# Optimization experiments

Measured on AMD Instinct MI355X. Metric: run time of the kernel, lower is better.

Reference implementation:

```python
import jax, jax.numpy as jnp
import numpy as np

N_PMTS = 12
N_TICKS = 550
BIN_SIGMA = 0.1
GAUSS_NORM = 1.0 / (BIN_SIGMA * 2.5066282746)
B, N_DEP, K = 8, 64, 512  # batch, depositions/event, electron slot cap per deposition


def setup_inputs() -> dict:
    key = jax.random.key(0)
    ks = jax.random.split(key, 10)
    # energy depositions [B, N, 4] = x, y, z, E(MeV)
    xy = jax.random.normal(ks[0], (B, N_DEP, 2), dtype=jnp.float32) * 5.0
    z = jax.random.uniform(ks[1], (B, N_DEP, 1), dtype=jnp.float32, minval=50.0, maxval=500.0)
    # E ~ 0.0115 MeV -> n = E*1e6/22.4 ~ up to ~513 electrons, capped at K
    E = jax.random.uniform(ks[2], (B, N_DEP, 1), dtype=jnp.float32, minval=0.002, maxval=0.0115)
    energy_depositions = jnp.concatenate([xy, z, E], axis=-1)
    return {
        "energy_depositions": energy_depositions,
        "e_draws": jax.random.normal(ks[3], (B, N_DEP), dtype=jnp.float32),
        "diff_draws": jax.random.normal(ks[4], (B, N_DEP, K, 3), dtype=jnp.float32),
        "unif_draws": jax.random.uniform(ks[5], (B, N_DEP, K), dtype=jnp.float32),
        "W1": jax.random.normal(ks[6], (2, 28), dtype=jnp.float32) * (1.0 / np.sqrt(2.0)),
        "b1": jnp.zeros((28,), dtype=jnp.float32),
        "W2": jax.random.normal(ks[7], (28, 12), dtype=jnp.float32) * (1.0 / np.sqrt(28.0)),
        "b2": jnp.zeros((12,), dtype=jnp.float32),
        "diffusion_scale": jnp.array([1.0, 1.0, 0.25], dtype=jnp.float32),
        "pmt_response_scale": jnp.ones((12,), dtype=jnp.float32),
        "lifetime": jnp.float32(25.0),
    }


def reference(energy_depositions, e_draws, diff_draws, unif_draws,
              W1, b1, W2, b2, diffusion_scale, pmt_response_scale, lifetime):
    dt = energy_depositions.dtype
    pos = energy_depositions[..., :3]            # [B,N,3]
    E = energy_depositions[..., 3]               # [B,N]
    # generate_electrons: n = E*1e6/22.4, sigma = sqrt(0.15 n)
    n = E * 1000.0 * 1000.0 / 22.4
    sigma = jnp.sqrt(0.15 * n)
    n_elec = jnp.clip((sigma * e_draws + n).astype(jnp.int32), 0, K)  # [B,N]
    slot_mask = jnp.arange(K)[None, None, :] < n_elec[..., None]       # [B,N,K]
    # diffuse_electrons: scale^2 * draw * sqrt(z) + position
    sqrt_z = jnp.sqrt(pos[..., 2])                                     # [B,N]
    elec = (diffusion_scale ** 2) * diff_draws * sqrt_z[..., None, None] + pos[:, :, None, :]  # [B,N,K,3]
    z_e = elec[..., 2]                                                 # [B,N,K]
    # apply_lifetime: accept with prob 1 - exp(-z/lifetime)
    prob = 1.0 - jnp.exp(-z_e / lifetime)
    mask = (slot_mask & (prob > unif_draws)).astype(dt)                # [B,N,K]
    # PMT response MLP on xy, scaled
    xy_e = elec[..., :2]
    h = jax.nn.sigmoid(xy_e @ W1 + b1)
    pmt = jax.nn.sigmoid(h @ W2 + b2) * (pmt_response_scale ** 2)      # [B,N,K,12]
    pmt = pmt * mask[..., None]
    # gaussian tick histogram over 550 ticks centered at 0.5..549.5
    ticks = jnp.arange(N_TICKS, dtype=dt) + 0.5
    g = GAUSS_NORM * jnp.exp(-((ticks - z_e[..., None]) ** 2) / BIN_SIGMA)  # [B,N,K,550]
    # sum over all electrons of the event: [B, 12, 550]
    return jnp.einsum('bnkp,bnkt->bpt', pmt, g)
```

## Files before the change

### kernel.cpp

```cpp
#include <hip/hip_runtime.h>
#include <hip/hip_fp16.h>

#define NB   8
#define NDEP 64
#define KK   512
#define NP   12
#define NT   550
#define L2E  1.4426950408889634f


static __device__ __forceinline__ float fast_rcp(float x) {
    return __builtin_amdgcn_rcpf(x);
}
static __device__ __forceinline__ unsigned packh2(float a, float b) {
    __half2 h = __floats2half2_rn(a, b);
    return __builtin_bit_cast(unsigned, h);
}

__global__ __launch_bounds__(256) void init_kernel(
    const float* __restrict__ W1, const float* __restrict__ b1,
    const float* __restrict__ W2, const float* __restrict__ b2,
    const float* __restrict__ pscale,
    float* __restrict__ ws, float* __restrict__ out, int out_size)
{
    const int idx = blockIdx.x * 256 + threadIdx.x;
    for (int i = idx; i < out_size; i += gridDim.x * 256) out[i] = 0.0f;

    if (blockIdx.x == 0) {
        const int t = threadIdx.x;
        if (t < 28) {
            ws[t]      = W1[t]      * L2E;
            ws[28 + t] = W1[28 + t] * L2E;
            ws[56 + t] = b1[t]      * L2E;
        }
        if (t >= 64 && t < 232) {
            const int e = t - 64, j = e / 6, c = e - j * 6;
            ((unsigned*)(ws + 84))[e] = packh2(W2[j * NP + 2 * c], W2[j * NP + 2 * c + 1]);
        }
        if (t >= 232 && t < 238) {
            const int c = t - 232;
            ((unsigned*)(ws + 252))[c] = packh2(b2[2 * c], b2[2 * c + 1]);
        }
        if (t >= 238 && t < 250) {
            const int p = t - 238;
            ws[258 + p] = pscale[p] * pscale[p] * 3.9894228040143274f;
        }
    }
}

template<int S>
static __device__ __forceinline__ void gather_reduce(
    const float* __restrict__ wl, int lane, int t_lo, int b,
    float* __restrict__ out)
{
    constexpr int W = 64 / S;
    const int tw  = lane & (W - 1);
    const int sub = lane / W;
    const float tc = (float)(t_lo + tw) + 0.5f;

    float acc[NP];
    #pragma unroll
    for (int p = 0; p < NP; ++p) acc[p] = 0.0f;

    #pragma unroll 4
    for (int i = 0; i < W; ++i) {
        const int k = sub * W + i;
        const int o = (k << 4) + ((k >> 4) << 2);
        const float4 r0 = *(const float4*)&wl[o];
        const float4 r1 = *(const float4*)&wl[o + 4];
        const float4 r2 = *(const float4*)&wl[o + 8];
        const float ez  = wl[o + 12];
        const float d   = tc - ez;
        const float g   = exp2f(-14.426950408889634f * d * d);
        acc[0]  = fmaf(r0.x, g, acc[0]);  acc[1]  = fmaf(r0.y, g, acc[1]);
        acc[2]  = fmaf(r0.z, g, acc[2]);  acc[3]  = fmaf(r0.w, g, acc[3]);
        acc[4]  = fmaf(r1.x, g, acc[4]);  acc[5]  = fmaf(r1.y, g, acc[5]);
        acc[6]  = fmaf(r1.z, g, acc[6]);  acc[7]  = fmaf(r1.w, g, acc[7]);
        acc[8]  = fmaf(r2.x, g, acc[8]);  acc[9]  = fmaf(r2.y, g, acc[9]);
        acc[10] = fmaf(r2.z, g, acc[10]); acc[11] = fmaf(r2.w, g, acc[11]);
    }

    #pragma unroll
    for (int msk = W; msk < 64; msk <<= 1) {
        #pragma unroll
        for (int p = 0; p < NP; ++p) acc[p] += __shfl_xor(acc[p], msk);
    }

    if (lane < W) {
        float* ob = out + ((size_t)b * NP) * NT + (t_lo + tw);
        #pragma unroll
        for (int p = 0; p < NP; ++p) atomicAdd(&ob[p * NT], acc[p]);
    }
}

__global__ __launch_bounds__(256) void next_sim_wave(
    const float* __restrict__ ed,
    const float* __restrict__ edraw,
    const float* __restrict__ ddraw,
    const float* __restrict__ udraw,
    const float* __restrict__ wst,
    const float* __restrict__ dscale, const float* __restrict__ life,
    float* __restrict__ out)
{
    __shared__ float lds[4][1040];

    const int tid  = threadIdx.x;
    const int lane = tid & 63;
    const int wid  = tid >> 6;
    const int bid  = blockIdx.x;
    const int bn   = bid >> 1;
    const int g    = ((bid & 1) << 2) | wid;
    const int b    = bn >> 6;

    const float4 dep  = ((const float4*)ed)[bn];
    const float nval  = dep.w * (1000000.0f / 22.4f);
    const float sigma = sqrtf(0.15f * nval);
    int ne = (int)(sigma * edraw[bn] + nval);
    ne = min(max(ne, 0), KK);
    const int k0 = g << 6;
    if (k0 >= ne) return;

    const float sqz     = sqrtf(dep.z);
    const float invLife = fast_rcp(life[0]);
    const float dS0 = dscale[0] * dscale[0];
    const float dS1 = dscale[1] * dscale[1];
    const float dS2 = dscale[2] * dscale[2];

    const int k = k0 + lane;
    const float* dd = ddraw + ((size_t)bn * KK + k) * 3;
    const float d0 = dd[0], d1 = dd[1], d2 = dd[2];
    const float ez = fmaf(dS2 * d2, sqz, dep.z);
    const float ex = fmaf(dS0 * d0, sqz, dep.x);
    const float ey = fmaf(dS1 * d1, sqz, dep.y);
    const float prob = 1.0f - __expf(-ez * invLife);
    const float m = ((k < ne) && (prob > udraw[(size_t)bn * KK + k])) ? 1.0f : 0.0f;

    const float*   w1a  = wst;
    const float*   w1b  = wst + 28;
    const float*   b1s  = wst + 56;
    const __half2* w2pk = (const __half2*)(wst + 84);
    const __half2* b2pk = (const __half2*)(wst + 252);
    const float*   qtab = wst + 258;

    __half2 pa0 = b2pk[0], pa1 = b2pk[1], pa2 = b2pk[2];
    __half2 pa3 = b2pk[3], pa4 = b2pk[4], pa5 = b2pk[5];
    #pragma unroll 4
    for (int j = 0; j < 28; ++j) {
        const float lg  = fmaf(w1a[j], ex, fmaf(w1b[j], ey, b1s[j]));
        const float hjf = fast_rcp(1.0f + exp2f(-lg));
        const __half2 h2 = __float2half2_rn(hjf);
        pa0 = __hfma2(h2, w2pk[j * 6 + 0], pa0);
        pa1 = __hfma2(h2, w2pk[j * 6 + 1], pa1);
        pa2 = __hfma2(h2, w2pk[j * 6 + 2], pa2);
        pa3 = __hfma2(h2, w2pk[j * 6 + 3], pa3);
        pa4 = __hfma2(h2, w2pk[j * 6 + 4], pa4);
        pa5 = __hfma2(h2, w2pk[j * 6 + 5], pa5);
    }
    float pm[NP];
    { float2 f;
      f = __half22float2(pa0); pm[0] = f.x; pm[1] = f.y;
      f = __half22float2(pa1); pm[2] = f.x; pm[3] = f.y;
      f = __half22float2(pa2); pm[4] = f.x; pm[5] = f.y;
      f = __half22float2(pa3); pm[6] = f.x; pm[7] = f.y;
      f = __half22float2(pa4); pm[8] = f.x; pm[9] = f.y;
      f = __half22float2(pa5); pm[10] = f.x; pm[11] = f.y; }

    float q[NP];
    #pragma unroll
    for (int p = 0; p < NP; ++p)
        q[p] = qtab[p] * m * fast_rcp(1.0f + exp2f(-pm[p] * L2E));

    float* wl = lds[wid];
    const int off = (lane << 4) + ((lane >> 4) << 2);
    *(float4*)&wl[off]     = make_float4(q[0], q[1],  q[2],  q[3]);
    *(float4*)&wl[off + 4] = make_float4(q[4], q[5],  q[6],  q[7]);
    *(float4*)&wl[off + 8] = make_float4(q[8], q[9],  q[10], q[11]);
    wl[off + 12] = ez;

    float ezmin = ez, ezmax = ez;
    #pragma unroll
    for (int msk = 1; msk < 64; msk <<= 1) {
        ezmin = fminf(ezmin, __shfl_xor(ezmin, msk));
        ezmax = fmaxf(ezmax, __shfl_xor(ezmax, msk));
    }
    const int fmin = (int)floorf(ezmin);
    const int fmax = (int)floorf(ezmax);
    const int need = fmax - fmin + 7;

    if (need <= 16) {
        const int t_lo = min(max(fmin - 3, 0), NT - 16);
        gather_reduce<4>(wl, lane, t_lo, b, out);
    } else {
        const int t_lo = min(max(fmin - 3, 0), NT - 32);
        gather_reduce<2>(wl, lane, t_lo, b, out);
    }
}

extern "C" void kernel_launch(void* const* d_in, const int* in_sizes, int n_in,
                              void* d_out, int out_size, void* d_ws, size_t ws_size,
                              hipStream_t stream) {
    const float* ed     = (const float*)d_in[0];
    const float* edraw  = (const float*)d_in[1];
    const float* ddraw  = (const float*)d_in[2];
    const float* udraw  = (const float*)d_in[3];
    const float* W1     = (const float*)d_in[4];
    const float* b1     = (const float*)d_in[5];
    const float* W2     = (const float*)d_in[6];
    const float* b2     = (const float*)d_in[7];
    const float* dscale = (const float*)d_in[8];
    const float* pscale = (const float*)d_in[9];
    const float* life   = (const float*)d_in[10];
    float* ws  = (float*)d_ws;
    float* out = (float*)d_out;

    init_kernel<<<64, 256, 0, stream>>>(W1, b1, W2, b2, pscale, ws, out, out_size);
    next_sim_wave<<<NB * NDEP * 2, 256, 0, stream>>>(
        ed, edraw, ddraw, udraw, ws, dscale, life, out);
}
```

Before: 20.66 us.

## Reduce per-deposition partials in LDS before global atomics, one block per deposition

```diff
diff --git a/kernel.cpp b/kernel.cpp
--- a/kernel.cpp
+++ b/kernel.cpp
@@ -6,6 +6,7 @@
 #define KK   512
 #define NP   12
 #define NT   550
+#define BWIN 40
 #define L2E  1.4426950408889634f
 
 
@@ -49,14 +50,14 @@
 }
 
 template<int S>
-static __device__ __forceinline__ void gather_reduce(
-    const float* __restrict__ wl, int lane, int t_lo, int b,
-    float* __restrict__ out)
+static __device__ __forceinline__ void gather_partial(
+    const float* __restrict__ wl, int lane, int t_lo, int off,
+    float* __restrict__ ppart)
 {
     constexpr int W = 64 / S;
     const int tw  = lane & (W - 1);
     const int sub = lane / W;
-    const float tc = (float)(t_lo + tw) + 0.5f;
+    const float tc = (float)t_lo + (float)tw + 0.5f;
 
     float acc[NP];
     #pragma unroll
@@ -87,13 +88,14 @@
     }
 
     if (lane < W) {
-        float* ob = out + ((size_t)b * NP) * NT + (t_lo + tw);
-        #pragma unroll
-        for (int p = 0; p < NP; ++p) atomicAdd(&ob[p * NT], acc[p]);
-    }
-}
-
-__global__ __launch_bounds__(256) void next_sim_wave(
+        float* pp = ppart + (size_t)(off + lane) * NP;
+        *(float4*)&pp[0] = make_float4(acc[0], acc[1],  acc[2],  acc[3]);
+        *(float4*)&pp[4] = make_float4(acc[4], acc[5],  acc[6],  acc[7]);
+        *(float4*)&pp[8] = make_float4(acc[8], acc[9],  acc[10], acc[11]);
+    }
+}
+
+__global__ __launch_bounds__(512) void next_sim_wave(
     const float* __restrict__ ed,
     const float* __restrict__ edraw,
     const float* __restrict__ ddraw,
@@ -102,97 +104,122 @@
     const float* __restrict__ dscale, const float* __restrict__ life,
     float* __restrict__ out)
 {
-    __shared__ float lds[4][1040];
+    __shared__ float rows[8][1040];
+    __shared__ float part[8][BWIN * NP];
+    __shared__ int2  hdr[8];
 
     const int tid  = threadIdx.x;
     const int lane = tid & 63;
     const int wid  = tid >> 6;
-    const int bid  = blockIdx.x;
-    const int bn   = bid >> 1;
-    const int g    = ((bid & 1) << 2) | wid;
+    const int bn   = blockIdx.x;
     const int b    = bn >> 6;
 
-    const float4 dep  = ((const float4*)ed)[bn];
+    const float4 dep = ((const float4*)ed)[bn];
+    const float  edr = edraw[bn];
+    const int    k   = (wid << 6) + lane;
+    const float* dd  = ddraw + ((size_t)bn * KK + k) * 3;
+    const float d0 = dd[0], d1 = dd[1], d2 = dd[2];
+    const float u  = udraw[(size_t)bn * KK + k];
+
     const float nval  = dep.w * (1000000.0f / 22.4f);
     const float sigma = sqrtf(0.15f * nval);
-    int ne = (int)(sigma * edraw[bn] + nval);
+    int ne = (int)(sigma * edr + nval);
     ne = min(max(ne, 0), KK);
-    const int k0 = g << 6;
-    if (k0 >= ne) return;
-
-    const float sqz     = sqrtf(dep.z);
-    const float invLife = fast_rcp(life[0]);
-    const float dS0 = dscale[0] * dscale[0];
-    const float dS1 = dscale[1] * dscale[1];
-    const float dS2 = dscale[2] * dscale[2];
-
-    const int k = k0 + lane;
-    const float* dd = ddraw + ((size_t)bn * KK + k) * 3;
-    const float d0 = dd[0], d1 = dd[1], d2 = dd[2];
-    const float ez = fmaf(dS2 * d2, sqz, dep.z);
-    const float ex = fmaf(dS0 * d0, sqz, dep.x);
-    const float ey = fmaf(dS1 * d1, sqz, dep.y);
-    const float prob = 1.0f - __expf(-ez * invLife);
-    const float m = ((k < ne) && (prob > udraw[(size_t)bn * KK + k])) ? 1.0f : 0.0f;
-
-    const float*   w1a  = wst;
-    const float*   w1b  = wst + 28;
-    const float*   b1s  = wst + 56;
-    const __half2* w2pk = (const __half2*)(wst + 84);
-    const __half2* b2pk = (const __half2*)(wst + 252);
-    const float*   qtab = wst + 258;
-
-    __half2 pa0 = b2pk[0], pa1 = b2pk[1], pa2 = b2pk[2];
-    __half2 pa3 = b2pk[3], pa4 = b2pk[4], pa5 = b2pk[5];
-    #pragma unroll 4
-    for (int j = 0; j < 28; ++j) {
-        const float lg  = fmaf(w1a[j], ex, fmaf(w1b[j], ey, b1s[j]));
-        const float hjf = fast_rcp(1.0f + exp2f(-lg));
-        const __half2 h2 = __float2half2_rn(hjf);
-        pa0 = __hfma2(h2, w2pk[j * 6 + 0], pa0);
-        pa1 = __hfma2(h2, w2pk[j * 6 + 1], pa1);
-        pa2 = __hfma2(h2, w2pk[j * 6 + 2], pa2);
-        pa3 = __hfma2(h2, w2pk[j * 6 + 3], pa3);
-        pa4 = __hfma2(h2, w2pk[j * 6 + 4], pa4);
-        pa5 = __hfma2(h2, w2pk[j * 6 + 5], pa5);
-    }
-    float pm[NP];
-    { float2 f;
-      f = __half22float2(pa0); pm[0] = f.x; pm[1] = f.y;
-      f = __half22float2(pa1); pm[2] = f.x; pm[3] = f.y;
-      f = __half22float2(pa2); pm[4] = f.x; pm[5] = f.y;
-      f = __half22float2(pa3); pm[6] = f.x; pm[7] = f.y;
-      f = __half22float2(pa4); pm[8] = f.x; pm[9] = f.y;
-      f = __half22float2(pa5); pm[10] = f.x; pm[11] = f.y; }
-
-    float q[NP];
-    #pragma unroll
-    for (int p = 0; p < NP; ++p)
-        q[p] = qtab[p] * m * fast_rcp(1.0f + exp2f(-pm[p] * L2E));
-
-    float* wl = lds[wid];
-    const int off = (lane << 4) + ((lane >> 4) << 2);
-    *(float4*)&wl[off]     = make_float4(q[0], q[1],  q[2],  q[3]);
-    *(float4*)&wl[off + 4] = make_float4(q[4], q[5],  q[6],  q[7]);
-    *(float4*)&wl[off + 8] = make_float4(q[8], q[9],  q[10], q[11]);
-    wl[off + 12] = ez;
-
-    float ezmin = ez, ezmax = ez;
-    #pragma unroll
-    for (int msk = 1; msk < 64; msk <<= 1) {
-        ezmin = fminf(ezmin, __shfl_xor(ezmin, msk));
-        ezmax = fmaxf(ezmax, __shfl_xor(ezmax, msk));
-    }
-    const int fmin = (int)floorf(ezmin);
-    const int fmax = (int)floorf(ezmax);
-    const int need = fmax - fmin + 7;
-
-    if (need <= 16) {
-        const int t_lo = min(max(fmin - 3, 0), NT - 16);
-        gather_reduce<4>(wl, lane, t_lo, b, out);
+    const int tb = (int)floorf(dep.z) - BWIN / 2;
+    const bool walive = ((wid << 6) < ne);
+
+    if (walive) {
+        const float sqz     = sqrtf(dep.z);
+        const float invLife = fast_rcp(life[0]);
+        const float dS0 = dscale[0] * dscale[0];
+        const float dS1 = dscale[1] * dscale[1];
+        const float dS2 = dscale[2] * dscale[2];
+
+        const float ez = fmaf(dS2 * d2, sqz, dep.z);
+        const float ex = fmaf(dS0 * d0, sqz, dep.x);
+        const float ey = fmaf(dS1 * d1, sqz, dep.y);
+        const float prob = 1.0f - __expf(-ez * invLife);
+        const float m = ((k < ne) && (prob > u)) ? 1.0f : 0.0f;
+
+        const float*   w1a  = wst;
+        const float*   w1b  = wst + 28;
+        const float*   b1s  = wst + 56;
+        const __half2* w2pk = (const __half2*)(wst + 84);
+        const __half2* b2pk = (const __half2*)(wst + 252);
+        const float*   qtab = wst + 258;
+
+        __half2 pa0 = b2pk[0], pa1 = b2pk[1], pa2 = b2pk[2];
+        __half2 pa3 = b2pk[3], pa4 = b2pk[4], pa5 = b2pk[5];
+        #pragma unroll 4
+        for (int j = 0; j < 28; ++j) {
+            const float lg  = fmaf(w1a[j], ex, fmaf(w1b[j], ey, b1s[j]));
+            const float hjf = fast_rcp(1.0f + exp2f(-lg));
+            const __half2 h2 = __float2half2_rn(hjf);
+            pa0 = __hfma2(h2, w2pk[j * 6 + 0], pa0);
+            pa1 = __hfma2(h2, w2pk[j * 6 + 1], pa1);
+            pa2 = __hfma2(h2, w2pk[j * 6 + 2], pa2);
+            pa3 = __hfma2(h2, w2pk[j * 6 + 3], pa3);
+            pa4 = __hfma2(h2, w2pk[j * 6 + 4], pa4);
+            pa5 = __hfma2(h2, w2pk[j * 6 + 5], pa5);
+        }
+        float pm[NP];
+        { float2 f;
+          f = __half22float2(pa0); pm[0] = f.x; pm[1] = f.y;
+          f = __half22float2(pa1); pm[2] = f.x; pm[3] = f.y;
+          f = __half22float2(pa2); pm[4] = f.x; pm[5] = f.y;
+          f = __half22float2(pa3); pm[6] = f.x; pm[7] = f.y;
+          f = __half22float2(pa4); pm[8] = f.x; pm[9] = f.y;
+          f = __half22float2(pa5); pm[10] = f.x; pm[11] = f.y; }
+
+        float q[NP];
+        #pragma unroll
+        for (int p = 0; p < NP; ++p)
+            q[p] = qtab[p] * m * fast_rcp(1.0f + exp2f(-pm[p] * L2E));
+
+        float* wl = rows[wid];
+        const int off = (lane << 4) + ((lane >> 4) << 2);
+        *(float4*)&wl[off]     = make_float4(q[0], q[1],  q[2],  q[3]);
+        *(float4*)&wl[off + 4] = make_float4(q[4], q[5],  q[6],  q[7]);
+        *(float4*)&wl[off + 8] = make_float4(q[8], q[9],  q[10], q[11]);
+        wl[off + 12] = ez;
+
+        float ezmin = ez, ezmax = ez;
+        #pragma unroll
+        for (int msk = 1; msk < 64; msk <<= 1) {
+            ezmin = fminf(ezmin, __shfl_xor(ezmin, msk));
+            ezmax = fmaxf(ezmax, __shfl_xor(ezmax, msk));
+        }
+        const int fmin = (int)floorf(ezmin);
+        const int fmax = (int)floorf(ezmax);
+        const int need = fmax - fmin + 7;
+
+        if (need <= 16) {
+            const int t_lo = min(max(fmin - 3, tb), tb + BWIN - 16);
+            gather_partial<4>(wl, lane, t_lo, t_lo - tb, part[wid]);
+            if (lane == 0) hdr[wid] = make_int2(t_lo - tb, 16);
+        } else {
+            const int t_lo = min(max(fmin - 3, tb), tb + BWIN - 32);
+            gather_partial<2>(wl, lane, t_lo, t_lo - tb, part[wid]);
+            if (lane == 0) hdr[wid] = make_int2(t_lo - tb, 32);
+        }
     } else {
-        const int t_lo = min(max(fmin - 3, 0), NT - 32);
-        gather_reduce<2>(wl, lane, t_lo, b, out);
+        if (lane == 0) hdr[wid] = make_int2(0, 0);
+    }
+    __syncthreads();
+
+    if (tid < BWIN * NP) {
+        const int t_rel = tid / NP;
+        const int p     = tid - t_rel * NP;
+        float s = 0.0f;
+        #pragma unroll
+        for (int w = 0; w < 8; ++w) {
+            const int2 h  = hdr[w];
+            const int  dt = t_rel - h.x;
+            if ((unsigned)dt < (unsigned)h.y)
+                s += part[w][t_rel * NP + p];
+        }
+        if (s != 0.0f)
+            atomicAdd(&out[((size_t)b * NP + p) * NT + (tb + t_rel)], s);
     }
 }
 
@@ -214,6 +241,6 @@
     float* out = (float*)d_out;
 
     init_kernel<<<64, 256, 0, stream>>>(W1, b1, W2, b2, pscale, ws, out, out_size);
-    next_sim_wave<<<NB * NDEP * 2, 256, 0, stream>>>(
+    next_sim_wave<<<NB * NDEP, 512, 0, stream>>>(
         ed, edraw, ddraw, udraw, ws, dscale, life, out);
 }
```

Measured after the change: 20.83 us. About the same (+0.8%).
